# Performance work log

Hardware: AMD Instinct MI355X
Metric: run time of the kernel (lower is better)

Reference implementation:

```python
import jax, jax.numpy as jnp
import numpy as np

HISTORY = 64
WINDOW = 32
DIM = 32
N_PATTERNS = 16
AMP = 2.0


def setup_inputs() -> dict:
    key = jax.random.key(0)
    ks = jax.random.split(key, 7)
    B, L = 128, 131072
    T = L // WINDOW  # 4096 scan steps
    x = jax.random.normal(ks[0], (B, L), jnp.float32)
    avg = jax.random.normal(ks[1], (B, N_PATTERNS), jnp.float32)
    avg_scores = avg - avg.mean(axis=-1, keepdims=True)
    noise = jax.random.normal(ks[2], (B, T, WINDOW), jnp.float32)
    # keys: xavier_uniform on (dim, n_patterns)
    kbound = float(np.sqrt(6.0 / (DIM + N_PATTERNS)))
    keys = jax.random.uniform(ks[3], (DIM, N_PATTERNS), jnp.float32, -kbound, kbound)
    # shapes = rand(n_patterns, 2) * amp * 2
    shapes = jax.random.uniform(ks[4], (N_PATTERNS, 2), jnp.float32) * (AMP * 2.0)
    # conv1d default init: uniform(-1/sqrt(fan_in), 1/sqrt(fan_in)), fan_in = 1*history
    cb = float(1.0 / np.sqrt(HISTORY))
    conv_w = jax.random.uniform(ks[5], (DIM, 1, HISTORY), jnp.float32, -cb, cb)
    conv_b = jax.random.uniform(ks[6], (DIM,), jnp.float32, -cb, cb)
    return {"x": x, "avg_scores": avg_scores, "noise": noise,
            "conv_w": conv_w, "conv_b": conv_b, "keys": keys, "shapes": shapes}


def reference(x, avg_scores, noise, conv_w, conv_b, keys, shapes):
    B, L = x.shape
    inv_p = 1.0 / N_PATTERNS
    # left-pad by history-1, conv1d(1 -> dim, kernel=history, stride=window) + relu
    padded = jnp.pad(x, ((0, 0), (HISTORY - 1, 0)))[:, None, :]  # [B,1,L+H-1]
    out = jax.lax.conv_general_dilated(
        padded, conv_w, window_strides=(WINDOW,), padding='VALID',
        dimension_numbers=('NCH', 'OIH', 'NCH'))  # [B,dim,T]
    out = jax.nn.relu(out + conv_b[None, :, None])
    out = out.transpose(2, 0, 1)  # [T,B,dim]
    # relu6 attention scores against pattern keys
    attn_scores = jnp.clip(jnp.einsum('tbd,dp->tbp', out, keys), 0.0, 6.0)  # [T,B,P]

    def step(avg, score):
        prob = jax.nn.softmax(score - avg, axis=-1)  # [B,P]
        return avg + prob - inv_p, prob

    _, probs = jax.lax.scan(step, avg_scores, attn_scores)  # probs: [T,B,P]
    attn_probs = probs.transpose(1, 0, 2)  # [B,T,P]
    shapeparams = jnp.einsum('btp,pc->btc', attn_probs, shapes)  # [B,T,2]
    offset = shapeparams[:, :, 0:1]  # broadcast over window
    std = shapeparams[:, :, 1:2]
    signal = (offset + noise * std).reshape(B, -1)[:, :L]  # [B,L]
    return jax.nn.relu(signal - x)
```

## Files before the change

kernel.cpp:

```cpp
#include <hip/hip_runtime.h>

static constexpr int BATCH = 128;
static constexpr int LEN   = 131072;
static constexpr int T     = 4096;
static constexpr int DIM   = 32;
static constexpr int NP    = 16;

static constexpr int NCHUNK = 64;
static constexpr int SPC    = T / NCHUNK;
static constexpr int WARM   = 128;

static constexpr int TT = 128;

#define L2E   1.44269504088896340736f
#define L2E16 (1.44269504088896340736f / 16.0f)

typedef __attribute__((ext_vector_type(8))) short  short8;
typedef __attribute__((ext_vector_type(4))) float  f32x4;

__device__ __forceinline__ float fexp2(float x) {
#if __has_builtin(__builtin_amdgcn_exp2f)
  return __builtin_amdgcn_exp2f(x);
#else
  return exp2f(x);
#endif
}

__device__ __forceinline__ float frcp(float x) {
#if __has_builtin(__builtin_amdgcn_rcpf)
  return __builtin_amdgcn_rcpf(x);
#else
  return 1.0f / x;
#endif
}

template <int CTRL>
__device__ __forceinline__ float dppf(float v) {
  return __int_as_float(
      __builtin_amdgcn_update_dpp(0, __float_as_int(v), CTRL, 0xf, 0xf, true));
}

__device__ __forceinline__ float sum16(float v) {
  v += dppf<0xB1>(v);
  v += dppf<0x4E>(v);
  v += dppf<0x141>(v);
  v += dppf<0x140>(v);
  return v;
}

__device__ __forceinline__ short bf16c(float f) {
  unsigned u = __float_as_uint(f);
  unsigned r = u + 0x7fffu + ((u >> 16) & 1u);
  return (short)(r >> 16);
}

__global__ void __launch_bounds__(64) prep_kernel(
    const float* __restrict__ conv_w, const float* __restrict__ conv_b,
    const float* __restrict__ keys, short* __restrict__ frags) {
  int l = threadIdx.x;
  int ln15 = l & 15, kg = l >> 4;
#pragma unroll
  for (int fn = 0; fn < 2; ++fn)
#pragma unroll
    for (int fk = 0; fk < 2; ++fk) {
      const float* wp = conv_w + (fn * 16 + ln15) * 64 + fk * 32 + kg * 8;
      short* dst = frags + ((fn * 2 + fk) * 64 + l) * 8;
#pragma unroll
      for (int j = 0; j < 8; ++j) dst[j] = bf16c(wp[j]);
    }
  short* kd = frags + (256 + l) * 8;
#pragma unroll
  for (int j = 0; j < 8; ++j) kd[j] = bf16c(keys[(kg * 8 + j) * NP + ln15]);
  float* bp = (float*)(frags + 2560);
  bp[2 * l]     = conv_b[ln15];
  bp[2 * l + 1] = conv_b[16 + ln15];
}

__global__ void __launch_bounds__(256) scores_kernel(
    const float* __restrict__ x, const short* __restrict__ frags,
    _Float16* __restrict__ scoresh) {
  __shared__ short lds[4][1728];

  int tid = threadIdx.x;
  int lane = tid & 63;
  int mt   = tid >> 6;
  int blk = blockIdx.x;
  int b  = blk >> 5;
  int bt = blk & 31;
  int t0 = bt * TT;
  int T0w = t0 + mt * 32;
  const float* xb = x + (size_t)b * LEN;
  short* xw = lds[mt];
  short* rl = lds[mt] + 1088;

  int gbase = 32 * T0w - 64 + 16 * lane;
  float f[17];
#pragma unroll
  for (int s = 0; s < 4; ++s) {
    int gi = gbase + 4 * s;
    float4 v = make_float4(0.f, 0.f, 0.f, 0.f);
    if (gi >= 0) v = *(const float4*)(xb + gi);
    f[4 * s]     = v.x; f[4 * s + 1] = v.y;
    f[4 * s + 2] = v.z; f[4 * s + 3] = v.w;
  }
  f[16] = (gbase + 16 >= 0) ? xb[gbase + 16] : 0.f;

  short8 w0, w1;
#pragma unroll
  for (int j = 0; j < 8; ++j) { w0[j] = bf16c(f[j + 1]); w1[j] = bf16c(f[j + 9]); }
  *(short8*)(&xw[16 * lane])     = w0;
  *(short8*)(&xw[16 * lane + 8]) = w1;
  if (lane > 0) xw[16 * lane - 1] = bf16c(f[0]);
  if (lane < 32)
    xw[1024 + lane] = bf16c(xb[32 * T0w + 961 + lane]);

  int ln15 = lane & 15;
  int kg   = lane >> 4;

  const short8* wf = (const short8*)frags;
  short8 bw00 = wf[0 * 64 + lane];
  short8 bw01 = wf[1 * 64 + lane];
  short8 bw10 = wf[2 * 64 + lane];
  short8 bw11 = wf[3 * 64 + lane];
  short8 bk   = wf[4 * 64 + lane];
  const float2* bp = (const float2*)(frags + 2560);
  float2 bias = bp[lane];

  _Float16* dstb = scoresh + (b & 3) * 16 + ln15;

#pragma unroll
  for (int st = 0; st < 2; ++st) {
    int tl = st * 16 + ln15;
    const short* ap = &xw[32 * tl];
    short8 a0 = *(const short8*)(ap + kg * 8);
    short8 a1 = *(const short8*)(ap + 32 + kg * 8);

    f32x4 acc0 = {0.f, 0.f, 0.f, 0.f};
    f32x4 acc1 = {0.f, 0.f, 0.f, 0.f};
    acc0 = __builtin_amdgcn_mfma_f32_16x16x32_bf16(a0, bw00, acc0, 0, 0, 0);
    acc0 = __builtin_amdgcn_mfma_f32_16x16x32_bf16(a1, bw01, acc0, 0, 0, 0);
    acc1 = __builtin_amdgcn_mfma_f32_16x16x32_bf16(a0, bw10, acc1, 0, 0, 0);
    acc1 = __builtin_amdgcn_mfma_f32_16x16x32_bf16(a1, bw11, acc1, 0, 0, 0);

#pragma unroll
    for (int r = 0; r < 4; ++r) {
      int trow = kg * 4 + r;
      rl[trow * 40 + ln15]      = bf16c(fmaxf(acc0[r] + bias.x, 0.f));
      rl[trow * 40 + 16 + ln15] = bf16c(fmaxf(acc1[r] + bias.y, 0.f));
    }
    short8 a2 = *(const short8*)(&rl[ln15 * 40 + kg * 8]);
    f32x4 acc2 = {0.f, 0.f, 0.f, 0.f};
    acc2 = __builtin_amdgcn_mfma_f32_16x16x32_bf16(a2, bk, acc2, 0, 0, 0);

#pragma unroll
    for (int r = 0; r < 4; ++r) {
      float s = fminf(fmaxf(acc2[r], 0.f), 6.f) * L2E;
      int t = T0w + st * 16 + kg * 4 + r;
      dstb[((size_t)(b >> 2) * T + t) * 64] = (_Float16)s;
    }
  }
}

__global__ void __launch_bounds__(64) scanout_kernel(
    const _Float16* __restrict__ scoresh, const float* __restrict__ avg0,
    const float* __restrict__ shapes, const float* __restrict__ x,
    const float* __restrict__ noise, float* __restrict__ out) {
  __shared__ float2 oslds[4][64];

  int lane = threadIdx.x;
  int g = blockIdx.x & 31;
  int c = blockIdx.x >> 5;
  int gid = g * 64 + lane;
  int p = lane & 15;
  int bl = lane >> 4;
  float A = avg0[gid] * L2E;
  float sh0 = shapes[2 * p];
  float sh1 = shapes[2 * p + 1];
  int w = min(WARM, c * SPC);
  int tbeg = c * SPC - w;
  const _Float16* sp = scoresh + ((size_t)g * T + tbeg) * 64 + lane;

  float q0 = (float)sp[0 * 64],  q1 = (float)sp[1 * 64];
  float q2 = (float)sp[2 * 64],  q3 = (float)sp[3 * 64];
  float q4 = (float)sp[4 * 64],  q5 = (float)sp[5 * 64];
  float q6 = (float)sp[6 * 64],  q7 = (float)sp[7 * 64];
  float q8 = (float)sp[8 * 64],  q9 = (float)sp[9 * 64];
  float qa = (float)sp[10 * 64], qb = (float)sp[11 * 64];
  float qc = (float)sp[12 * 64], qd = (float)sp[13 * 64];
  float qe = (float)sp[14 * 64], qf = (float)sp[15 * 64];
  sp += 16 * 64;

#define WSTEP(Q)                                   \
  do {                                             \
    float e = fexp2(Q - A);                        \
    float r = sum16(e);                            \
    A = fmaf(e * L2E, frcp(r), A - L2E16);         \
    Q = (float)sp[0];                              \
    sp += 64;                                      \
  } while (0)

  for (int i = 0; i < w; i += 16) {
    WSTEP(q0); WSTEP(q1); WSTEP(q2); WSTEP(q3);
    WSTEP(q4); WSTEP(q5); WSTEP(q6); WSTEP(q7);
    WSTEP(q8); WSTEP(q9); WSTEP(qa); WSTEP(qb);
    WSTEP(qc); WSTEP(qd); WSTEP(qe); WSTEP(qf);
  }

#define CSTEP(Q, idx)                              \
  do {                                             \
    float e = fexp2(Q - A);                        \
    float r  = sum16(e);                           \
    float u0 = sum16(e * sh0);                     \
    float u1 = sum16(e * sh1);                     \
    float rc = frcp(r);                            \
    A = fmaf(e * L2E, rc, A - L2E16);              \
    if (p == 0) oslds[bl][idx] = make_float2(u0 * rc, u1 * rc); \
    Q = (float)sp[0];                              \
    sp += 64;                                      \
  } while (0)

  for (int i = 0; i < SPC; i += 16) {
    CSTEP(q0, i + 0);  CSTEP(q1, i + 1);  CSTEP(q2, i + 2);  CSTEP(q3, i + 3);
    CSTEP(q4, i + 4);  CSTEP(q5, i + 5);  CSTEP(q6, i + 6);  CSTEP(q7, i + 7);
    CSTEP(q8, i + 8);  CSTEP(q9, i + 9);  CSTEP(qa, i + 10); CSTEP(qb, i + 11);
    CSTEP(qc, i + 12); CSTEP(qd, i + 13); CSTEP(qe, i + 14); CSTEP(qf, i + 15);
  }
#undef WSTEP
#undef CSTEP

  size_t base = (size_t)(g * 4) * LEN + (size_t)c * 2048;
#pragma unroll
  for (int bb = 0; bb < 4; ++bb) {
    const float* xp = x     + base + (size_t)bb * LEN;
    const float* np = noise + base + (size_t)bb * LEN;
    float*       op = out   + base + (size_t)bb * LEN;
    float4 xv[8], nv[8];
#pragma unroll
    for (int k = 0; k < 8; ++k) {
      xv[k] = *(const float4*)(xp + (k * 64 + lane) * 4);
      nv[k] = *(const float4*)(np + (k * 64 + lane) * 4);
    }
#pragma unroll
    for (int k = 0; k < 8; ++k) {
      float2 os = oslds[bb][k * 8 + (lane >> 3)];
      float4 o;
      o.x = fmaxf(fmaf(nv[k].x, os.y, os.x) - xv[k].x, 0.f);
      o.y = fmaxf(fmaf(nv[k].y, os.y, os.x) - xv[k].y, 0.f);
      o.z = fmaxf(fmaf(nv[k].z, os.y, os.x) - xv[k].z, 0.f);
      o.w = fmaxf(fmaf(nv[k].w, os.y, os.x) - xv[k].w, 0.f);
      *(float4*)(op + (k * 64 + lane) * 4) = o;
    }
  }
}

extern "C" void kernel_launch(void* const* d_in, const int* in_sizes, int n_in,
                              void* d_out, int out_size, void* d_ws, size_t ws_size,
                              hipStream_t stream) {
  const float* x      = (const float*)d_in[0];
  const float* avg0   = (const float*)d_in[1];
  const float* noise  = (const float*)d_in[2];
  const float* conv_w = (const float*)d_in[3];
  const float* conv_b = (const float*)d_in[4];
  const float* keys   = (const float*)d_in[5];
  const float* shapes = (const float*)d_in[6];
  float* out = (float*)d_out;

  _Float16* scoresh = (_Float16*)d_ws;
  short* frags = (short*)((char*)d_ws + ((size_t)T * BATCH * NP * 2 + 4096));

  prep_kernel<<<1, 64, 0, stream>>>(conv_w, conv_b, keys, frags);
  scores_kernel<<<BATCH * (T / TT), 256, 0, stream>>>(x, frags, scoresh);
  scanout_kernel<<<32 * NCHUNK, 64, 0, stream>>>(scoresh, avg0, shapes, x, noise, out);
}
```

Baseline: 71.17 us.

## Prefetch noise tile into LDS via async global_load_lds during scan

Issues asynchronous global-to-LDS loads of this block's noise tile (32 KB) before the serial softmax scan starts, then waits on vmcnt before the output stage and reads noise from LDS. The goal is to hide noise-load latency behind the latency-bound scan so the epilogue only has to stream x and write out. It costs 32 KB of LDS per 64-thread block, which may reduce occupancy, and the scan's own score loads now share the vmcnt counter with the outstanding bulk loads.

```diff
diff --git a/kernel.cpp b/kernel.cpp
--- a/kernel.cpp
+++ b/kernel.cpp
@@ -52,6 +52,12 @@
   unsigned u = __float_as_uint(f);
   unsigned r = u + 0x7fffu + ((u >> 16) & 1u);
   return (short)(r >> 16);
+}
+
+__device__ __forceinline__ void g2lds16(const float* g, float* l) {
+  __builtin_amdgcn_global_load_lds(
+      (const __attribute__((address_space(1))) void*)g,
+      (__attribute__((address_space(3))) void*)l, 16, 0, 0);
 }
 
 __global__ void __launch_bounds__(64) prep_kernel(
@@ -165,6 +171,7 @@
     const _Float16* __restrict__ scoresh, const float* __restrict__ avg0,
     const float* __restrict__ shapes, const float* __restrict__ x,
     const float* __restrict__ noise, float* __restrict__ out) {
+  __shared__ float nslds[8192];
   __shared__ float2 oslds[4][64];
 
   int lane = threadIdx.x;
@@ -190,6 +197,15 @@
   float qe = (float)sp[14 * 64], qf = (float)sp[15 * 64];
   sp += 16 * 64;
 
+  size_t base = (size_t)(g * 4) * LEN + (size_t)c * 2048;
+#pragma unroll
+  for (int inst = 0; inst < 32; ++inst) {
+    int bb = inst >> 3, k = inst & 7;
+    g2lds16(noise + base + (size_t)bb * LEN + k * 256 + lane * 4,
+            &nslds[inst * 256]);
+  }
+  __builtin_amdgcn_sched_barrier(0);
+
 #define WSTEP(Q)                                   \
   do {                                             \
     float e = fexp2(Q - A);                        \
@@ -228,27 +244,26 @@
 #undef WSTEP
 #undef CSTEP
 
-  size_t base = (size_t)(g * 4) * LEN + (size_t)c * 2048;
+  asm volatile("s_waitcnt vmcnt(0)" ::: "memory");
+
 #pragma unroll
   for (int bb = 0; bb < 4; ++bb) {
-    const float* xp = x     + base + (size_t)bb * LEN;
-    const float* np = noise + base + (size_t)bb * LEN;
-    float*       op = out   + base + (size_t)bb * LEN;
-    float4 xv[8], nv[8];
+    const float* xp = x   + base + (size_t)bb * LEN;
+    float*       op = out + base + (size_t)bb * LEN;
+    float4 xv[8];
+#pragma unroll
+    for (int k = 0; k < 8; ++k)
+      xv[k] = *(const float4*)(xp + k * 256 + lane * 4);
 #pragma unroll
     for (int k = 0; k < 8; ++k) {
-      xv[k] = *(const float4*)(xp + (k * 64 + lane) * 4);
-      nv[k] = *(const float4*)(np + (k * 64 + lane) * 4);
-    }
-#pragma unroll
-    for (int k = 0; k < 8; ++k) {
+      float4 nv = *(const float4*)&nslds[(bb * 8 + k) * 256 + lane * 4];
       float2 os = oslds[bb][k * 8 + (lane >> 3)];
       float4 o;
-      o.x = fmaxf(fmaf(nv[k].x, os.y, os.x) - xv[k].x, 0.f);
-      o.y = fmaxf(fmaf(nv[k].y, os.y, os.x) - xv[k].y, 0.f);
-      o.z = fmaxf(fmaf(nv[k].z, os.y, os.x) - xv[k].z, 0.f);
-      o.w = fmaxf(fmaf(nv[k].w, os.y, os.x) - xv[k].w, 0.f);
-      *(float4*)(op + (k * 64 + lane) * 4) = o;
+      o.x = fmaxf(fmaf(nv.x, os.y, os.x) - xv[k].x, 0.f);
+      o.y = fmaxf(fmaf(nv.y, os.y, os.x) - xv[k].y, 0.f);
+      o.z = fmaxf(fmaf(nv.z, os.y, os.x) - xv[k].z, 0.f);
+      o.w = fmaxf(fmaf(nv.w, os.y, os.x) - xv[k].w, 0.f);
+      *(float4*)(op + k * 256 + lane * 4) = o;
     }
   }
 }
```

Measured after the change: 75.49 us. 1.06x slower.
